# Performance work log

Hardware: AMD Instinct MI355X
Metric: run time of the kernel (lower is better)

Reference implementation:

```python
import jax, jax.numpy as jnp
import numpy as np

NUM_EXPERTS = 8
TOP_K = 2
HIDDEN = 1024
NUM_TOKENS = 8192


def setup_inputs() -> dict:
    key = jax.random.key(0)
    k1, k2, k3 = jax.random.split(key, 3)
    x = jax.random.normal(k1, (NUM_TOKENS, HIDDEN), dtype=jnp.float32)
    # gate: nn.Linear(hidden, num_experts, bias=False) -> weight [E, H]
    gate_w = jax.random.normal(k2, (NUM_EXPERTS, HIDDEN), dtype=jnp.float32) * 0.02
    # experts: nn.Linear(hidden, hidden, bias=False) stacked -> [E, H_out, H_in]
    expert_w = jax.random.normal(k3, (NUM_EXPERTS, HIDDEN, HIDDEN), dtype=jnp.float32) * 0.02
    return {"x": x, "gate_w": gate_w, "expert_w": expert_w}


def reference(x, gate_w, expert_w):
    # --- routing ---
    logits = jnp.einsum("th,eh->te", x, gate_w)          # [T, E]
    probs = jax.nn.softmax(logits, axis=-1)
    weights, indices = jax.lax.top_k(probs, TOP_K)        # [T, K], [T, K]

    # --- expert compute (equivalent of dispatch + per-expert GEMM) ---
    # y_e = x @ W_e^T for every expert; tokens then gather their top-k rows.
    all_y = jnp.einsum("td,ehd->eth", x, expert_w)        # [E, T, H]

    # --- weighted combine (gather by routed expert ids) ---
    t_idx = jnp.arange(x.shape[0])[None, :]               # [1, T]
    y_sel = all_y[indices.T, t_idx, :]                    # [K, T, H]
    out = jnp.einsum("tk,kth->th", weights, y_sel)        # [T, H]
    return out
```

## Files before the change

kernel.cpp:

```cpp
#include <hip/hip_runtime.h>
#include <hip/hip_bf16.h>
#include <stdint.h>

#define NUM_TOKENS 8192
#define HIDDEN 1024
#define NEXP 8
#define TOPK 2

typedef __bf16 bf16;
typedef __bf16 bf16x4 __attribute__((ext_vector_type(4)));
typedef __bf16 bf16x8 __attribute__((ext_vector_type(8)));
typedef float f32x4 __attribute__((ext_vector_type(4)));

__device__ __forceinline__ void gld_lds16(const void* g, void* l) {
  __builtin_amdgcn_global_load_lds(
      (const __attribute__((address_space(1))) void*)(uintptr_t)g,
      (__attribute__((address_space(3))) void*)(uint32_t)(uintptr_t)l,
      16, 0, 0);
}

__global__ __launch_bounds__(256) void gate_route_kernel(
    const float* __restrict__ x, const float* __restrict__ gw,
    bf16* __restrict__ xbf, int* __restrict__ echoice, float* __restrict__ pchoice)
{
  const int wid  = threadIdx.x >> 6;
  const int lane = threadIdx.x & 63;
  const int t = blockIdx.x * 4 + wid;

  const float* xrow = x + (size_t)t * HIDDEN;
  bf16* xbrow = xbf + (size_t)t * HIDDEN;

  float acc[NEXP];
#pragma unroll
  for (int e = 0; e < NEXP; ++e) acc[e] = 0.f;

#pragma unroll
  for (int it = 0; it < 4; ++it) {
    const int idx = it * 256 + lane * 4;
    float4 xv = *(const float4*)(xrow + idx);
    bf16x4 xb;
    xb[0] = (bf16)xv.x; xb[1] = (bf16)xv.y; xb[2] = (bf16)xv.z; xb[3] = (bf16)xv.w;
    *(bf16x4*)(xbrow + idx) = xb;
#pragma unroll
    for (int e = 0; e < NEXP; ++e) {
      float4 gv = *(const float4*)(gw + e * HIDDEN + idx);
      acc[e] += xv.x * gv.x + xv.y * gv.y + xv.z * gv.z + xv.w * gv.w;
    }
  }
#pragma unroll
  for (int e = 0; e < NEXP; ++e) {
#pragma unroll
    for (int off = 32; off > 0; off >>= 1)
      acc[e] += __shfl_xor(acc[e], off, 64);
  }

  if (lane == 0) {
    float m = acc[0];
#pragma unroll
    for (int e = 1; e < NEXP; ++e) m = fmaxf(m, acc[e]);
    float p[NEXP]; float s = 0.f;
#pragma unroll
    for (int e = 0; e < NEXP; ++e) { p[e] = expf(acc[e] - m); s += p[e]; }
    const float inv = 1.f / s;
#pragma unroll
    for (int e = 0; e < NEXP; ++e) p[e] *= inv;
    int i0 = 0; float p0 = p[0];
#pragma unroll
    for (int e = 1; e < NEXP; ++e) if (p[e] > p0) { p0 = p[e]; i0 = e; }
    int i1 = -1; float p1 = -1.f;
#pragma unroll
    for (int e = 0; e < NEXP; ++e) if (e != i0 && p[e] > p1) { p1 = p[e]; i1 = e; }

    echoice[t]              = i0;
    echoice[NUM_TOKENS + t] = i1;
    pchoice[t]              = p0;
    pchoice[NUM_TOKENS + t] = p1;
  }
}

__global__ __launch_bounds__(1024) void build_lists_kernel(
    const int* __restrict__ echoice, const float* __restrict__ pchoice,
    int* __restrict__ cnt, int* __restrict__ tok, float* __restrict__ wt)
{
  const int tid  = threadIdx.x;
  const int wave = tid >> 6;
  const int lane = tid & 63;
  const int k = wave >> 3;
  const int w = wave & 7;
  const int tbase = w * 1024;

  const int*   ec = echoice + k * NUM_TOKENS;
  const float* pc = pchoice + k * NUM_TOKENS;

  __shared__ int wcnt[2][8][NEXP];
  __shared__ int woff[2][8][NEXP];

  const unsigned long long lower = ((unsigned long long)1 << lane) - 1;

  int   ev[16];
  float pv[16];
#pragma unroll
  for (int c = 0; c < 16; ++c) {
    ev[c] = ec[tbase + c * 64 + lane];
    pv[c] = pc[tbase + c * 64 + lane];
  }

  int cl[NEXP];
#pragma unroll
  for (int e = 0; e < NEXP; ++e) cl[e] = 0;
#pragma unroll
  for (int c = 0; c < 16; ++c) {
#pragma unroll
    for (int l = 0; l < NEXP; ++l)
      cl[l] += __popcll(__ballot(ev[c] == l));
  }
  if (lane < NEXP) wcnt[k][w][lane] = cl[lane];
  __syncthreads();

  if (lane < NEXP) {
    int off = 0;
#pragma unroll
    for (int ww = 0; ww < 8; ++ww) {
      if (ww == w) woff[k][w][lane] = off;
      off += wcnt[k][ww][lane];
    }
    if (w == 0) cnt[k * NEXP + lane] = off;
  }
  __syncthreads();

  int run[NEXP];
#pragma unroll
  for (int e = 0; e < NEXP; ++e) run[e] = woff[k][w][e];
#pragma unroll
  for (int c = 0; c < 16; ++c) {
    const int e = ev[c];
    int pos = 0;
#pragma unroll
    for (int l = 0; l < NEXP; ++l) {
      const unsigned long long m = __ballot(ev[c] == l);
      if (e == l) pos = run[l] + __popcll(m & lower);
      run[l] += __popcll(m);
    }
    const int list = k * NEXP + e;
    tok[(size_t)list * NUM_TOKENS + pos] = tbase + c * 64 + lane;
    wt [(size_t)list * NUM_TOKENS + pos] = pv[c];
  }
}

__global__ __launch_bounds__(256) void convert_w_kernel(
    const float* __restrict__ w, bf16* __restrict__ wbf)
{
  const size_t i = ((size_t)blockIdx.x * 256 + threadIdx.x) * 4;
  float4 v = *(const float4*)(w + i);
  bf16x4 b;
  b[0] = (bf16)v.x; b[1] = (bf16)v.y; b[2] = (bf16)v.z; b[3] = (bf16)v.w;
  *(bf16x4*)(wbf + i) = b;
}

template <int PASS>
__global__ __launch_bounds__(256) void moe_gemm_kernel(
    const bf16* __restrict__ xbf, const bf16* __restrict__ wbf,
    const int* __restrict__ cnt, const int* __restrict__ tok,
    const float* __restrict__ wt, float* __restrict__ out)
{
  const int id   = blockIdx.x;
  const int xcd  = id & 7;
  const int rr_  = id >> 3;
  const int nt   = rr_ & 7;
  const int pair = (rr_ >> 3) * 8 + xcd;
  const int e    = pair >> 6;
  const int mt   = pair & 63;

  const int list = PASS * NEXP + e;
  const int count = cnt[list];
  const int m0 = mt * 128;
  if (m0 >= count) return;
  const int rows = min(128, count - m0);

  __shared__ __align__(16) bf16 As[128 * 32];
  __shared__ __align__(16) bf16 Bs[128 * 32];
  __shared__ int   tok_s[128];
  __shared__ float wt_s[128];

  const int tid = threadIdx.x;
  if (tid < 128) {
    if (tid < rows) {
      tok_s[tid] = tok[(size_t)list * NUM_TOKENS + m0 + tid];
      wt_s[tid]  = wt [(size_t)list * NUM_TOKENS + m0 + tid];
    } else { tok_s[tid] = 0; wt_s[tid] = 0.f; }
  }
  __syncthreads();

  const int rr    = tid >> 2;
  const int cslot = tid & 3;
  const int c     = cslot ^ (rr & 3);
  const bf16* gA0 = xbf + (size_t)tok_s[rr] * HIDDEN + c * 8;
  const bf16* gA1 = xbf + (size_t)tok_s[64 + rr] * HIDDEN + c * 8;
  const bf16* gB0 = wbf + (size_t)e * HIDDEN * HIDDEN
                  + (size_t)(nt * 128 + rr) * HIDDEN + c * 8;
  const bf16* gB1 = gB0 + (size_t)64 * HIDDEN;
  bf16* lA = As + tid * 8;
  bf16* lB = Bs + tid * 8;

  const int wid  = tid >> 6;
  const int lane = tid & 63;
  const int wm = (wid >> 1) * 64;
  const int wn = (wid & 1) * 64;
  const int qm = lane & 15;
  const int cx = ((lane >> 4) ^ (qm & 3)) * 8;

  f32x4 acc[4][4];
#pragma unroll
  for (int i = 0; i < 4; ++i)
#pragma unroll
    for (int j = 0; j < 4; ++j) acc[i][j] = (f32x4){0.f, 0.f, 0.f, 0.f};

  for (int kc = 0; kc < HIDDEN; kc += 32) {
    gld_lds16(gA0 + kc, lA);
    gld_lds16(gA1 + kc, lA + 64 * 32);
    gld_lds16(gB0 + kc, lB);
    gld_lds16(gB1 + kc, lB + 64 * 32);
    __syncthreads();

    bf16x8 a[4], b[4];
#pragma unroll
    for (int i = 0; i < 4; ++i)
      a[i] = *(const bf16x8*)(As + (wm + i * 16 + qm) * 32 + cx);
#pragma unroll
    for (int j = 0; j < 4; ++j)
      b[j] = *(const bf16x8*)(Bs + (wn + j * 16 + qm) * 32 + cx);
#pragma unroll
    for (int i = 0; i < 4; ++i)
#pragma unroll
      for (int j = 0; j < 4; ++j)
        acc[i][j] = __builtin_amdgcn_mfma_f32_16x16x32_bf16(a[i], b[j], acc[i][j], 0, 0, 0);
    __syncthreads();
  }

  const int h0 = nt * 128 + wn + (lane & 15);
#pragma unroll
  for (int i = 0; i < 4; ++i) {
    const int rbase = wm + i * 16 + (lane >> 4) * 4;
#pragma unroll
    for (int r = 0; r < 4; ++r) {
      const int rl = rbase + r;
      if (rl < rows) {
        const int t = tok_s[rl];
        const float w = wt_s[rl];
        float* orow = out + (size_t)t * HIDDEN + h0;
#pragma unroll
        for (int j = 0; j < 4; ++j) {
          const float v = w * acc[i][j][r];
          if (PASS == 0) orow[j * 16] = v;
          else           orow[j * 16] += v;
        }
      }
    }
  }
}

extern "C" void kernel_launch(void* const* d_in, const int* in_sizes, int n_in,
                              void* d_out, int out_size, void* d_ws, size_t ws_size,
                              hipStream_t stream) {
  const float* x  = (const float*)d_in[0];
  const float* gw = (const float*)d_in[1];
  const float* ew = (const float*)d_in[2];
  float* out = (float*)d_out;

  char* ws = (char*)d_ws;
  int*   cnt     = (int*)ws;
  int*   echoice = (int*)(ws + 256);
  float* pchoice = (float*)(ws + 256 + (size_t)2 * NUM_TOKENS * 4);
  int*   tok = (int*)(ws + 256 + (size_t)4 * NUM_TOKENS * 4);
  float* wt  = (float*)(ws + 256 + (size_t)20 * NUM_TOKENS * 4);
  bf16*  xbf = (bf16*)(ws + 256 + (size_t)36 * NUM_TOKENS * 4);
  bf16*  wbf = (bf16*)((char*)xbf + (size_t)NUM_TOKENS * HIDDEN * 2);

  gate_route_kernel<<<NUM_TOKENS / 4, 256, 0, stream>>>(x, gw, xbf, echoice, pchoice);
  build_lists_kernel<<<1, 1024, 0, stream>>>(echoice, pchoice, cnt, tok, wt);
  convert_w_kernel<<<(NEXP * HIDDEN * HIDDEN) / (4 * 256), 256, 0, stream>>>(ew, wbf);

  moe_gemm_kernel<0><<<4096, 256, 0, stream>>>(xbf, wbf, cnt, tok, wt, out);
  moe_gemm_kernel<1><<<4096, 256, 0, stream>>>(xbf, wbf, cnt, tok, wt, out);
}
```

Baseline: 220.5 us.

## Merge two MoE GEMM passes into one atomic-accumulate launch and fix LDS swizzle

Replaces the two sequential per-top-k GEMM launches with a single 3D-grid launch covering both routing slots. The output is zeroed with a memset and accumulated via unsafe atomic adds. The LDS xor swizzle now keys on row pairs to avoid bank conflicts for 64-byte rows. The XCD-aware block remapping is dropped, which may reduce L2 locality, and atomics plus the memset add memory traffic.

```diff
diff --git a/kernel.cpp b/kernel.cpp
--- a/kernel.cpp
+++ b/kernel.cpp
@@ -157,21 +157,15 @@
   *(bf16x4*)(wbf + i) = b;
 }
 
-template <int PASS>
 __global__ __launch_bounds__(256) void moe_gemm_kernel(
     const bf16* __restrict__ xbf, const bf16* __restrict__ wbf,
     const int* __restrict__ cnt, const int* __restrict__ tok,
     const float* __restrict__ wt, float* __restrict__ out)
 {
-  const int id   = blockIdx.x;
-  const int xcd  = id & 7;
-  const int rr_  = id >> 3;
-  const int nt   = rr_ & 7;
-  const int pair = (rr_ >> 3) * 8 + xcd;
-  const int e    = pair >> 6;
-  const int mt   = pair & 63;
-
-  const int list = PASS * NEXP + e;
+  const int list = blockIdx.z;
+  const int mt = blockIdx.y;
+  const int nt = blockIdx.x;
+  const int e = list & 7;
   const int count = cnt[list];
   const int m0 = mt * 128;
   if (m0 >= count) return;
@@ -193,7 +187,7 @@
 
   const int rr    = tid >> 2;
   const int cslot = tid & 3;
-  const int c     = cslot ^ (rr & 3);
+  const int c     = cslot ^ ((rr >> 1) & 3);
   const bf16* gA0 = xbf + (size_t)tok_s[rr] * HIDDEN + c * 8;
   const bf16* gA1 = xbf + (size_t)tok_s[64 + rr] * HIDDEN + c * 8;
   const bf16* gB0 = wbf + (size_t)e * HIDDEN * HIDDEN
@@ -207,7 +201,7 @@
   const int wm = (wid >> 1) * 64;
   const int wn = (wid & 1) * 64;
   const int qm = lane & 15;
-  const int cx = ((lane >> 4) ^ (qm & 3)) * 8;
+  const int swz8 = (((lane >> 4) ^ ((qm >> 1) & 3))) * 8;
 
   f32x4 acc[4][4];
 #pragma unroll
@@ -225,10 +219,10 @@
     bf16x8 a[4], b[4];
 #pragma unroll
     for (int i = 0; i < 4; ++i)
-      a[i] = *(const bf16x8*)(As + (wm + i * 16 + qm) * 32 + cx);
+      a[i] = *(const bf16x8*)(As + (wm + i * 16 + qm) * 32 + swz8);
 #pragma unroll
     for (int j = 0; j < 4; ++j)
-      b[j] = *(const bf16x8*)(Bs + (wn + j * 16 + qm) * 32 + cx);
+      b[j] = *(const bf16x8*)(Bs + (wn + j * 16 + qm) * 32 + swz8);
 #pragma unroll
     for (int i = 0; i < 4; ++i)
 #pragma unroll
@@ -249,11 +243,8 @@
         const float w = wt_s[rl];
         float* orow = out + (size_t)t * HIDDEN + h0;
 #pragma unroll
-        for (int j = 0; j < 4; ++j) {
-          const float v = w * acc[i][j][r];
-          if (PASS == 0) orow[j * 16] = v;
-          else           orow[j * 16] += v;
-        }
+        for (int j = 0; j < 4; ++j)
+          unsafeAtomicAdd(&orow[j * 16], w * acc[i][j][r]);
       }
     }
   }
@@ -276,10 +267,11 @@
   bf16*  xbf = (bf16*)(ws + 256 + (size_t)36 * NUM_TOKENS * 4);
   bf16*  wbf = (bf16*)((char*)xbf + (size_t)NUM_TOKENS * HIDDEN * 2);
 
+  hipMemsetAsync(out, 0, (size_t)out_size * sizeof(float), stream);
   gate_route_kernel<<<NUM_TOKENS / 4, 256, 0, stream>>>(x, gw, xbf, echoice, pchoice);
   build_lists_kernel<<<1, 1024, 0, stream>>>(echoice, pchoice, cnt, tok, wt);
   convert_w_kernel<<<(NEXP * HIDDEN * HIDDEN) / (4 * 256), 256, 0, stream>>>(ew, wbf);
 
-  moe_gemm_kernel<0><<<4096, 256, 0, stream>>>(xbf, wbf, cnt, tok, wt, out);
-  moe_gemm_kernel<1><<<4096, 256, 0, stream>>>(xbf, wbf, cnt, tok, wt, out);
-}
+  dim3 grid(HIDDEN / 128, NUM_TOKENS / 128, 2 * NEXP);
+  moe_gemm_kernel<<<grid, 256, 0, stream>>>(xbf, wbf, cnt, tok, wt, out);
+}
```

New measurement: 232.2 us. +5.3%, slower.
